# Kernel tuning notes

Measured on AMD Instinct MI355X. Metric: run time of the kernel, lower is better.

The kernel has to match this reference:

```python
import jax, jax.numpy as jnp
import numpy as np

D, N_EXP, N_TOK = 2048, 8, 32768


def setup_inputs() -> dict:
    key = jax.random.key(0)
    k_h, k_eps, k_ww, k_bw, k_wn, k_bn = jax.random.split(key, 6)
    bound = 1.0 / np.sqrt(D)  # nn.Linear default init range
    return {
        "h": jax.random.normal(k_h, (N_TOK, D), dtype=jnp.float32),
        "W_w": jax.random.uniform(k_ww, (D, N_EXP), jnp.float32, -bound, bound),
        "b_w": jax.random.uniform(k_bw, (N_EXP,), jnp.float32, -bound, bound),
        "W_n": jax.random.uniform(k_wn, (D, N_EXP), jnp.float32, -bound, bound),
        "b_n": jax.random.uniform(k_bn, (N_EXP,), jnp.float32, -bound, bound),
        "eps": jax.random.normal(k_eps, (N_TOK, N_EXP), dtype=jnp.float32),
        "top_k": 2,
    }


def reference(h, W_w, b_w, W_n, b_n, eps, top_k):
    # logits = lin_w(h); noise_scale = softplus(lin_noise(h))
    logits = jnp.einsum("td,de->te", h, W_w) + b_w          # [T, E]
    noise = eps * jax.nn.softplus(jnp.einsum("td,de->te", h, W_n) + b_n)
    noisy = logits + noise                                   # [T, E]
    full = jax.nn.softmax(noisy, axis=-1)
    topk_vals, ix = jax.lax.top_k(noisy, top_k)              # [T, k]
    # scatter topk values into -inf tensor == mask non-topk with -inf
    mask = jax.nn.one_hot(ix, noisy.shape[-1], dtype=jnp.bool_).any(axis=-2)  # [T, E]
    sparse = jnp.where(mask, noisy, -jnp.inf)
    return jax.nn.softmax(sparse, axis=-1), ix, full
```

## Files before the change

### kernel.cpp

```cpp
#include <hip/hip_runtime.h>
#include <math.h>

constexpr int D_DIM = 2048;
constexpr int NEXP  = 8;
constexpr int NTOK  = 32768;
constexpr int TT    = 4;
constexpr int KC    = 128;
constexpr int NCH   = D_DIM / KC;
constexpr int WPB   = 4;

constexpr int KGSTR = 33;
constexpr int MSTR  = 32 * KGSTR;
constexpr int BSTR  = 2 * MSTR;

typedef float vf4 __attribute__((ext_vector_type(4)));

__device__ __forceinline__ float softplus_f(float x) {
    return (x > 20.0f) ? x : log1pf(expf(x));
}

__global__ __launch_bounds__(256, 4)
void noisy_topk_router(const float* __restrict__ h,
                       const float* __restrict__ Ww,
                       const float* __restrict__ bw,
                       const float* __restrict__ Wn,
                       const float* __restrict__ bn,
                       const float* __restrict__ eps,
                       float* __restrict__ out_sparse,
                       float* __restrict__ out_ix,
                       float* __restrict__ out_full)
{
    __shared__ float sW[2 * BSTR];

    const int tid  = threadIdx.x;
    const int lane = tid & 63;
    const int wave = tid >> 6;
    const int t0   = (blockIdx.x * WPB + wave) * TT;
    const int role = lane & 1;
    const int kg   = lane >> 1;

    const int s_kg   = tid >> 3;
    const int s_slot = tid & 7;
    const int s_dst0 = 0 * MSTR + (s_kg & 31) * KGSTR + s_slot * 4;
    const int s_dst1 = 1 * MSTR + (s_kg & 31) * KGSTR + s_slot * 4;
    const int s_src  = (tid & 255) * 4;

    float p[TT * 8];
#pragma unroll
    for (int i = 0; i < TT * 8; ++i) p[i] = 0.0f;

    const float* hbase = h + (size_t)t0 * D_DIM + 4 * kg;

    {
        vf4 a = *(const vf4*)(Ww + s_src);
        vf4 b = *(const vf4*)(Wn + s_src);
#pragma unroll
        for (int i = 0; i < 4; ++i) sW[s_dst0 + i] = a[i];
#pragma unroll
        for (int i = 0; i < 4; ++i) sW[s_dst1 + i] = b[i];
    }
    vf4 hv[TT];
#pragma unroll
    for (int t = 0; t < TT; ++t)
        hv[t] = *(const vf4*)(hbase + (size_t)t * D_DIM);
    __syncthreads();

#pragma unroll 1
    for (int c = 0; c < NCH; ++c) {
        const int cur = c & 1;
        const bool more = (c + 1 < NCH);

        vf4 wa, wb;
        if (more) {
            const int src = (c + 1) * (KC * NEXP) + s_src;
            wa = *(const vf4*)(Ww + src);
            wb = *(const vf4*)(Wn + src);
        }
        vf4 hvn[TT];
        if (more) {
#pragma unroll
            for (int t = 0; t < TT; ++t)
                hvn[t] = *(const vf4*)(hbase + (size_t)t * D_DIM + (c + 1) * KC);
        }

        const int rbase = cur * BSTR + role * MSTR + kg * KGSTR;
        float w[32];
#pragma unroll
        for (int j = 0; j < 32; ++j) w[j] = sW[rbase + j];

#pragma unroll
        for (int t = 0; t < TT; ++t) {
#pragma unroll
            for (int r = 0; r < 4; ++r) {
                const float x = hv[t][r];
#pragma unroll
                for (int o = 0; o < 8; ++o)
                    p[t * 8 + o] = fmaf(x, w[r * 8 + o], p[t * 8 + o]);
            }
        }

        if (more) {
            const int obase = (cur ^ 1) * BSTR;
#pragma unroll
            for (int i = 0; i < 4; ++i) sW[obase + s_dst0 + i] = wa[i];
#pragma unroll
            for (int i = 0; i < 4; ++i) sW[obase + s_dst1 + i] = wb[i];
#pragma unroll
            for (int t = 0; t < TT; ++t) hv[t] = hvn[t];
        }
        __syncthreads();
    }

#pragma unroll
    for (int s = 0; s < 5; ++s) {
        const int m = 2 << s;
        const bool hi = (lane & m) != 0;
        const int n = 32 >> (s + 1);
#pragma unroll
        for (int j = 0; j < n; ++j) {
            float a  = p[2 * j];
            float b  = p[2 * j + 1];
            float ta = __shfl_xor(a, m, 64);
            float tb = __shfl_xor(b, m, 64);
            p[j] = hi ? (b + tb) : (a + ta);
        }
    }

    const int  o         = (lane >> 1) & 7;
    const bool noiseLane = (role != 0);
    const int  tok       = t0 + (lane >> 4);
    const float bias     = noiseLane ? bn[o] : bw[o];

    const float val = p[0] + bias;
    const float sp  = softplus_f(val);
    const float spN = __shfl_xor(sp, 1, 64);
    const float ev  = eps[(size_t)tok * NEXP + o];
    const float noisy = val + ev * spN;

    float v0 = noisy; int i0 = o;
#pragma unroll
    for (int m = 2; m <= 8; m <<= 1) {
        float ov = __shfl_xor(v0, m, 64);
        int   oi = __shfl_xor(i0, m, 64);
        bool take = (ov > v0) || (ov == v0 && oi < i0);
        v0 = take ? ov : v0;
        i0 = take ? oi : i0;
    }
    float v1 = (o == i0) ? -INFINITY : noisy; int i1 = o;
#pragma unroll
    for (int m = 2; m <= 8; m <<= 1) {
        float ov = __shfl_xor(v1, m, 64);
        int   oi = __shfl_xor(i1, m, 64);
        bool take = (ov > v1) || (ov == v1 && oi < i1);
        v1 = take ? ov : v1;
        i1 = take ? oi : i1;
    }
    const float ex = expf(noisy - v0);
    float ssum = ex;
#pragma unroll
    for (int m = 2; m <= 8; m <<= 1) ssum += __shfl_xor(ssum, m, 64);
    const float fullv = ex / ssum;
    const float dd  = expf(v1 - v0);
    const float den = 1.0f + dd;
    const float sparsev = (o == i0) ? (1.0f / den)
                        : (o == i1) ? (dd / den) : 0.0f;

    if (!noiseLane) {
        out_sparse[(size_t)tok * NEXP + o] = sparsev;
        out_full  [(size_t)tok * NEXP + o] = fullv;
        if (o == 0) {
            out_ix[(size_t)tok * 2]     = (float)i0;
            out_ix[(size_t)tok * 2 + 1] = (float)i1;
        }
    }
}

extern "C" void kernel_launch(void* const* d_in, const int* in_sizes, int n_in,
                              void* d_out, int out_size, void* d_ws, size_t ws_size,
                              hipStream_t stream) {
    const float* h   = (const float*)d_in[0];
    const float* Ww  = (const float*)d_in[1];
    const float* bw  = (const float*)d_in[2];
    const float* Wn  = (const float*)d_in[3];
    const float* bn  = (const float*)d_in[4];
    const float* eps = (const float*)d_in[5];

    float* out_sparse = (float*)d_out;
    float* out_ix     = out_sparse + (size_t)NTOK * NEXP;
    float* out_full   = out_ix + (size_t)NTOK * 2;

    const int grid = NTOK / (TT * WPB);
    noisy_topk_router<<<grid, 256, 0, stream>>>(h, Ww, bw, Wn, bn, eps,
                                                out_sparse, out_ix, out_full);
}
```

Before: 370.3 us.

## Read router weights directly from global memory instead of LDS staging

Drops the double-buffered shared-memory staging of the two weight matrices and the per-chunk __syncthreads. Each lane now loads its 32 weights per chunk straight from global memory (relying on L1/L2 caching of the small 128 KB weight set), and the chunk loop is fully unrolled. This removes barrier and LDS traffic, but adds redundant global/cache loads per wave, loses the explicit prefetch of the next chunk, and increases code size and register pressure.

```diff
diff --git a/kernel.cpp b/kernel.cpp
--- a/kernel.cpp
+++ b/kernel.cpp
@@ -8,10 +8,6 @@
 constexpr int KC    = 128;
 constexpr int NCH   = D_DIM / KC;
 constexpr int WPB   = 4;
-
-constexpr int KGSTR = 33;
-constexpr int MSTR  = 32 * KGSTR;
-constexpr int BSTR  = 2 * MSTR;
 
 typedef float vf4 __attribute__((ext_vector_type(4)));
 
@@ -30,8 +26,6 @@
                        float* __restrict__ out_ix,
                        float* __restrict__ out_full)
 {
-    __shared__ float sW[2 * BSTR];
-
     const int tid  = threadIdx.x;
     const int lane = tid & 63;
     const int wave = tid >> 6;
@@ -39,54 +33,25 @@
     const int role = lane & 1;
     const int kg   = lane >> 1;
 
-    const int s_kg   = tid >> 3;
-    const int s_slot = tid & 7;
-    const int s_dst0 = 0 * MSTR + (s_kg & 31) * KGSTR + s_slot * 4;
-    const int s_dst1 = 1 * MSTR + (s_kg & 31) * KGSTR + s_slot * 4;
-    const int s_src  = (tid & 255) * 4;
+    const float* Wm    = role ? Wn : Ww;
+    const float* wbase = Wm + kg * 32;
+    const float* hbase = h + (size_t)t0 * D_DIM + 4 * kg;
 
     float p[TT * 8];
 #pragma unroll
     for (int i = 0; i < TT * 8; ++i) p[i] = 0.0f;
 
-    const float* hbase = h + (size_t)t0 * D_DIM + 4 * kg;
+#pragma unroll
+    for (int c = 0; c < NCH; ++c) {
+        vf4 wv[8];
+#pragma unroll
+        for (int q = 0; q < 8; ++q)
+            wv[q] = *(const vf4*)(wbase + c * (KC * NEXP) + q * 4);
 
-    {
-        vf4 a = *(const vf4*)(Ww + s_src);
-        vf4 b = *(const vf4*)(Wn + s_src);
+        vf4 hv[TT];
 #pragma unroll
-        for (int i = 0; i < 4; ++i) sW[s_dst0 + i] = a[i];
-#pragma unroll
-        for (int i = 0; i < 4; ++i) sW[s_dst1 + i] = b[i];
-    }
-    vf4 hv[TT];
-#pragma unroll
-    for (int t = 0; t < TT; ++t)
-        hv[t] = *(const vf4*)(hbase + (size_t)t * D_DIM);
-    __syncthreads();
-
-#pragma unroll 1
-    for (int c = 0; c < NCH; ++c) {
-        const int cur = c & 1;
-        const bool more = (c + 1 < NCH);
-
-        vf4 wa, wb;
-        if (more) {
-            const int src = (c + 1) * (KC * NEXP) + s_src;
-            wa = *(const vf4*)(Ww + src);
-            wb = *(const vf4*)(Wn + src);
-        }
-        vf4 hvn[TT];
-        if (more) {
-#pragma unroll
-            for (int t = 0; t < TT; ++t)
-                hvn[t] = *(const vf4*)(hbase + (size_t)t * D_DIM + (c + 1) * KC);
-        }
-
-        const int rbase = cur * BSTR + role * MSTR + kg * KGSTR;
-        float w[32];
-#pragma unroll
-        for (int j = 0; j < 32; ++j) w[j] = sW[rbase + j];
+        for (int t = 0; t < TT; ++t)
+            hv[t] = *(const vf4*)(hbase + (size_t)t * D_DIM + c * KC);
 
 #pragma unroll
         for (int t = 0; t < TT; ++t) {
@@ -94,21 +59,12 @@
             for (int r = 0; r < 4; ++r) {
                 const float x = hv[t][r];
 #pragma unroll
-                for (int o = 0; o < 8; ++o)
-                    p[t * 8 + o] = fmaf(x, w[r * 8 + o], p[t * 8 + o]);
+                for (int o = 0; o < 8; ++o) {
+                    const int j = r * 8 + o;
+                    p[t * 8 + o] = fmaf(x, wv[j >> 2][j & 3], p[t * 8 + o]);
+                }
             }
         }
-
-        if (more) {
-            const int obase = (cur ^ 1) * BSTR;
-#pragma unroll
-            for (int i = 0; i < 4; ++i) sW[obase + s_dst0 + i] = wa[i];
-#pragma unroll
-            for (int i = 0; i < 4; ++i) sW[obase + s_dst1 + i] = wb[i];
-#pragma unroll
-            for (int t = 0; t < TT; ++t) hv[t] = hvn[t];
-        }
-        __syncthreads();
     }
 
 #pragma unroll
```

After: 462.2 us. 1.25x slower.
